# Kernel optimization log

Measured on AMD Instinct MI355X. Metric: run time of the kernel, lower is better.

The kernel has to match this reference:

```python
import jax, jax.numpy as jnp
import numpy as np

DIM = 4096
K = 16  # 2**bits, bits=4
SCALE = 1.0 / DIM ** 0.5
# Lloyd-Max optimal 16-level quantizer centroids for N(0,1)
LLOYD_MAX_4BIT = np.array([
    -2.7326, -2.0690, -1.6181, -1.2562, -0.9424, -0.6568, -0.3881, -0.1284,
     0.1284,  0.3881,  0.6568,  0.9424,  1.2562,  1.6181,  2.0690,  2.7326,
], dtype=np.float32)


def setup_inputs() -> dict:
    key = jax.random.key(0)
    k_x, k_q = jax.random.split(key)
    x = jax.random.normal(k_x, (2048, DIM), dtype=jnp.float32)
    # Random orthogonal rotation via QR, matching torch.linalg.qr(randn(dim, dim))
    g = jax.random.normal(k_q, (DIM, DIM), dtype=jnp.float32)
    rotation, _ = jnp.linalg.qr(g)
    codebook = jnp.asarray(LLOYD_MAX_4BIT)
    return {"x": x, "rotation": rotation, "codebook": codebook}


def reference(x, rotation, codebook):
    # x: (N, dim); rotation: (dim, dim) orthogonal; codebook: (K,)
    shape = x.shape
    x_flat = x.reshape(-1, DIM).astype(jnp.float32)
    y = x_flat @ rotation.T                      # (N, dim) rotate
    y_norm = y / SCALE                           # coords ~ N(0, 1)
    # (N, dim, K) distance tensor -> argmin over codebook axis
    dists = jnp.abs(y_norm[..., None] - codebook)
    idx = jnp.argmin(dists, axis=-1)             # (N, dim) int32
    y_hat = codebook[idx] * SCALE                # gather + rescale
    x_hat = y_hat @ rotation                     # inverse rotation
    return x_hat.reshape(shape)
```

## Files before the change

### kernel.cpp

```cpp
#include <hip/hip_runtime.h>
#include <hip/hip_bf16.h>


typedef __attribute__((ext_vector_type(8))) _Float16 f16x8;
typedef __attribute__((ext_vector_type(4))) float f32x4;

__device__ __forceinline__ unsigned short f2h(float f) {
    _Float16 h = (_Float16)f;
    return *reinterpret_cast<unsigned short*>(&h);
}

__device__ __forceinline__ float quant16(float yn, const float* c) {
    float v = c[0];
#pragma unroll
    for (int i = 0; i < 15; i++) {
        const float bnd = 0.5f * (c[i] + c[i + 1]);
        v = (yn > bnd) ? c[i + 1] : v;
    }
    return v;
}

__global__ __launch_bounds__(256) void convert_x_kernel(
    const float* __restrict__ x, unsigned short* __restrict__ xb) {
    const int i = (blockIdx.x * 256 + threadIdx.x) * 4;
    float4 v = *reinterpret_cast<const float4*>(x + i);
    ushort4 b;
    b.x = f2h(v.x); b.y = f2h(v.y); b.z = f2h(v.z); b.w = f2h(v.w);
    *reinterpret_cast<ushort4*>(xb + i) = b;
}

__global__ __launch_bounds__(256) void conv_rot_kernel(
    const float* __restrict__ R, unsigned short* __restrict__ Rb,
    unsigned short* __restrict__ Rt) {
    __shared__ float t[64][65];
    const int tid = threadIdx.x;
    const int tr = blockIdx.y * 64, tc = blockIdx.x * 64;
    const int r0 = tid >> 4;
    const int c4 = (tid & 15) << 2;
#pragma unroll
    for (int i = 0; i < 4; i++) {
        const int r = r0 + i * 16;
        float4 v = *reinterpret_cast<const float4*>(
            &R[(size_t)(tr + r) * 4096 + tc + c4]);
        ushort4 b;
        b.x = f2h(v.x); b.y = f2h(v.y); b.z = f2h(v.z); b.w = f2h(v.w);
        *reinterpret_cast<ushort4*>(&Rb[(size_t)(tr + r) * 4096 + tc + c4]) = b;
        t[r][c4 + 0] = v.x; t[r][c4 + 1] = v.y;
        t[r][c4 + 2] = v.z; t[r][c4 + 3] = v.w;
    }
    __syncthreads();
#pragma unroll
    for (int i = 0; i < 16; i++) {
        const int idx = tid + 256 * i;
        const int rr = idx >> 6;
        const int cc = idx & 63;
        Rt[(size_t)(tc + rr) * 4096 + tr + cc] = f2h(t[cc][rr]);
    }
}

constexpr int GK = 4096;
constexpr int BM = 128, BN = 256, BK = 64;
constexpr int NT = GK / BK;
constexpr int A_LDS = BM * BK * 2;
constexpr int BUF = (BM + BN) * BK * 2;
constexpr int LDS_DYN = 2 * BUF;

template <bool QUANT>
__global__ __launch_bounds__(768, 3) void gemm_nt_kernel(
    const unsigned short* __restrict__ A, const unsigned short* __restrict__ Bt,
    void* __restrict__ Cout, const float* __restrict__ cb16) {
    extern __shared__ char smem[];
    const int tid = threadIdx.x;
    const int lane = tid & 63;
    const int w = tid >> 6;

    const int bid = blockIdx.x;
    const int wgid = (bid & 7) * 32 + (bid >> 3);
    const int tn = wgid & 15;
    const int tm = wgid >> 4;

    if (w >= 8) {
        const int tp = tid - 512;
        const int pw = tp >> 6;
        const int prow = tp >> 3;
        const int pcol = (((tp & 7) ^ (prow & 7)) << 3);
        const unsigned short* P[12];
#pragma unroll
        for (int r = 0; r < 12; r++) {
            const int rir = r * 32 + prow;
            P[r] = (rir < BM)
                ? A + (size_t)(tm * BM + rir) * GK + pcol
                : Bt + (size_t)(tn * BN + (rir - BM)) * GK + pcol;
        }
#pragma unroll
        for (int r = 0; r < 12; r++) {
            __builtin_amdgcn_global_load_lds(
                (const __attribute__((address_space(1))) void*)P[r],
                (__attribute__((address_space(3))) void*)(
                    smem + r * 4096 + pw * 1024), 16, 0, 0);
            P[r] += BK;
        }
        asm volatile("s_waitcnt vmcnt(0)" ::: "memory");
        __builtin_amdgcn_s_barrier();
        __builtin_amdgcn_sched_barrier(0);
        int wb = BUF;
        for (int t = 0; t < NT; ++t) {
            if (t + 1 < NT) {
#pragma unroll
                for (int r = 0; r < 12; r++) {
                    __builtin_amdgcn_global_load_lds(
                        (const __attribute__((address_space(1))) void*)P[r],
                        (__attribute__((address_space(3))) void*)(
                            smem + wb + r * 4096 + pw * 1024), 16, 0, 0);
                    P[r] += BK;
                }
            }
            asm volatile("s_waitcnt vmcnt(0)" ::: "memory");
            __builtin_amdgcn_s_barrier();
            __builtin_amdgcn_sched_barrier(0);
            wb ^= BUF;
        }
        return;
    }

    const int wm = w >> 2;
    const int wn = w & 3;

    f32x4 acc[4][4];
#pragma unroll
    for (int m = 0; m < 4; m++)
#pragma unroll
        for (int n = 0; n < 4; n++) acc[m][n] = (f32x4){0.f, 0.f, 0.f, 0.f};

    const int frow = lane & 15;
    const int sw0 = (((lane >> 4) ^ (frow & 7)) << 4);
    const int sw1 = (((4 + (lane >> 4)) ^ (frow & 7)) << 4);
    const int arow = (wm * 64 + frow) * 128;
    const int brow = A_LDS + (wn * 64 + frow) * 128;

#define LDA(m, sw) (*reinterpret_cast<const f16x8*>(smem + lb + arow + (m) * 2048 + (sw)))
#define LDB(n, sw) (*reinterpret_cast<const f16x8*>(smem + lb + brow + (n) * 2048 + (sw)))
#define MFMA16(A0, A1, A2, A3, B0, B1, B2, B3)                                     \
    acc[0][0] = __builtin_amdgcn_mfma_f32_16x16x32_f16(A0, B0, acc[0][0], 0, 0, 0); \
    acc[0][1] = __builtin_amdgcn_mfma_f32_16x16x32_f16(A0, B1, acc[0][1], 0, 0, 0); \
    acc[0][2] = __builtin_amdgcn_mfma_f32_16x16x32_f16(A0, B2, acc[0][2], 0, 0, 0); \
    acc[0][3] = __builtin_amdgcn_mfma_f32_16x16x32_f16(A0, B3, acc[0][3], 0, 0, 0); \
    acc[1][0] = __builtin_amdgcn_mfma_f32_16x16x32_f16(A1, B0, acc[1][0], 0, 0, 0); \
    acc[1][1] = __builtin_amdgcn_mfma_f32_16x16x32_f16(A1, B1, acc[1][1], 0, 0, 0); \
    acc[1][2] = __builtin_amdgcn_mfma_f32_16x16x32_f16(A1, B2, acc[1][2], 0, 0, 0); \
    acc[1][3] = __builtin_amdgcn_mfma_f32_16x16x32_f16(A1, B3, acc[1][3], 0, 0, 0); \
    acc[2][0] = __builtin_amdgcn_mfma_f32_16x16x32_f16(A2, B0, acc[2][0], 0, 0, 0); \
    acc[2][1] = __builtin_amdgcn_mfma_f32_16x16x32_f16(A2, B1, acc[2][1], 0, 0, 0); \
    acc[2][2] = __builtin_amdgcn_mfma_f32_16x16x32_f16(A2, B2, acc[2][2], 0, 0, 0); \
    acc[2][3] = __builtin_amdgcn_mfma_f32_16x16x32_f16(A2, B3, acc[2][3], 0, 0, 0); \
    acc[3][0] = __builtin_amdgcn_mfma_f32_16x16x32_f16(A3, B0, acc[3][0], 0, 0, 0); \
    acc[3][1] = __builtin_amdgcn_mfma_f32_16x16x32_f16(A3, B1, acc[3][1], 0, 0, 0); \
    acc[3][2] = __builtin_amdgcn_mfma_f32_16x16x32_f16(A3, B2, acc[3][2], 0, 0, 0); \
    acc[3][3] = __builtin_amdgcn_mfma_f32_16x16x32_f16(A3, B3, acc[3][3], 0, 0, 0);

    __builtin_amdgcn_s_barrier();
    __builtin_amdgcn_sched_barrier(0);

    int lb = 0;
    for (int t = 0; t < NT; ++t) {
        f16x8 a00, a01, a02, a03, b00, b01, b02, b03;
        f16x8 a10, a11, a12, a13, b10, b11, b12, b13;
        a00 = LDA(0, sw0); a01 = LDA(1, sw0); a02 = LDA(2, sw0); a03 = LDA(3, sw0);
        b00 = LDB(0, sw0); b01 = LDB(1, sw0); b02 = LDB(2, sw0); b03 = LDB(3, sw0);
        a10 = LDA(0, sw1); a11 = LDA(1, sw1); a12 = LDA(2, sw1); a13 = LDA(3, sw1);
        b10 = LDB(0, sw1); b11 = LDB(1, sw1); b12 = LDB(2, sw1); b13 = LDB(3, sw1);
        asm volatile("s_waitcnt lgkmcnt(8)" ::: "memory");
        __builtin_amdgcn_sched_barrier(0);
        __builtin_amdgcn_s_setprio(1);
        MFMA16(a00, a01, a02, a03, b00, b01, b02, b03)
        __builtin_amdgcn_s_setprio(0);
        asm volatile("s_waitcnt lgkmcnt(0)" ::: "memory");
        __builtin_amdgcn_sched_barrier(0);
        __builtin_amdgcn_s_setprio(1);
        MFMA16(a10, a11, a12, a13, b10, b11, b12, b13)
        __builtin_amdgcn_s_setprio(0);
        __builtin_amdgcn_s_barrier();
        __builtin_amdgcn_sched_barrier(0);
        lb ^= BUF;
    }
#undef LDA
#undef LDB
#undef MFMA16

    const int crow0 = tm * BM + wm * 64 + ((lane >> 4) << 2);
    const int ccol0 = tn * BN + wn * 64 + frow;
    if constexpr (QUANT) {
        float c[16];
#pragma unroll
        for (int i = 0; i < 16; i++) c[i] = cb16[i];
        unsigned short* O = (unsigned short*)Cout;
#pragma unroll
        for (int m = 0; m < 4; m++)
#pragma unroll
            for (int n = 0; n < 4; n++)
#pragma unroll
                for (int j = 0; j < 4; j++)
                    O[(size_t)(crow0 + m * 16 + j) * 4096 + ccol0 + n * 16] =
                        f2h(quant16(acc[m][n][j] * 64.0f, c) * 0.015625f);
    } else {
        float* O = (float*)Cout;
#pragma unroll
        for (int m = 0; m < 4; m++)
#pragma unroll
            for (int n = 0; n < 4; n++)
#pragma unroll
                for (int j = 0; j < 4; j++)
                    O[(size_t)(crow0 + m * 16 + j) * 4096 + ccol0 + n * 16] =
                        acc[m][n][j];
    }
}

extern "C" void kernel_launch(void* const* d_in, const int* in_sizes, int n_in,
                              void* d_out, int out_size, void* d_ws,
                              size_t ws_size, hipStream_t stream) {
    const float* x = (const float*)d_in[0];
    const float* rot = (const float*)d_in[1];
    const float* cb = (const float*)d_in[2];
    float* out = (float*)d_out;

    unsigned short* Xh = (unsigned short*)d_ws;
    unsigned short* Rh = Xh + (size_t)2048 * 4096;
    unsigned short* Rt = Rh + (size_t)4096 * 4096;
    unsigned short* Yh = Rt + (size_t)4096 * 4096;

    (void)hipFuncSetAttribute(
        reinterpret_cast<const void*>(&gemm_nt_kernel<true>),
        hipFuncAttributeMaxDynamicSharedMemorySize, LDS_DYN);
    (void)hipFuncSetAttribute(
        reinterpret_cast<const void*>(&gemm_nt_kernel<false>),
        hipFuncAttributeMaxDynamicSharedMemorySize, LDS_DYN);

    convert_x_kernel<<<8192, 256, 0, stream>>>(x, Xh);
    conv_rot_kernel<<<dim3(64, 64), 256, 0, stream>>>(rot, Rh, Rt);
    gemm_nt_kernel<true><<<256, 768, LDS_DYN, stream>>>(Xh, Rh, (void*)Yh, cb);
    gemm_nt_kernel<false><<<256, 768, LDS_DYN, stream>>>(Yh, Rt, (void*)out, nullptr);
}
```

Before: 170.0 us.

## Triple-buffer LDS stages and prefetch next tile's fragments across barrier

The producer waves now keep two K-tiles in flight using three LDS buffers instead of two. The consumer waves load the first half-fragments of the next tile into registers before the barrier, so LDS read latency overlaps with MFMA work. This raises dynamic LDS use by half, to about 144KB per block, which may limit occupancy under the 3-block launch bound. It also adds register pressure from the extra fragment sets.

```diff
diff --git a/kernel.cpp b/kernel.cpp
--- a/kernel.cpp
+++ b/kernel.cpp
@@ -63,7 +63,7 @@
 constexpr int NT = GK / BK;
 constexpr int A_LDS = BM * BK * 2;
 constexpr int BUF = (BM + BN) * BK * 2;
-constexpr int LDS_DYN = 2 * BUF;
+constexpr int LDS_DYN = 3 * BUF;
 
 template <bool QUANT>
 __global__ __launch_bounds__(768, 3) void gemm_nt_kernel(
@@ -92,34 +92,31 @@
                 ? A + (size_t)(tm * BM + rir) * GK + pcol
                 : Bt + (size_t)(tn * BN + (rir - BM)) * GK + pcol;
         }
-#pragma unroll
-        for (int r = 0; r < 12; r++) {
-            __builtin_amdgcn_global_load_lds(
-                (const __attribute__((address_space(1))) void*)P[r],
-                (__attribute__((address_space(3))) void*)(
-                    smem + r * 4096 + pw * 1024), 16, 0, 0);
-            P[r] += BK;
+#define PSTAGE(dstbase)                                                        \
+        {                                                                      \
+            _Pragma("unroll")                                                  \
+            for (int r = 0; r < 12; r++) {                                     \
+                __builtin_amdgcn_global_load_lds(                              \
+                    (const __attribute__((address_space(1))) void*)P[r],       \
+                    (__attribute__((address_space(3))) void*)(                 \
+                        smem + (dstbase) + r * 4096 + pw * 1024), 16, 0, 0);   \
+                P[r] += BK;                                                    \
+            }                                                                  \
         }
+        PSTAGE(0)
+        PSTAGE(BUF)
         asm volatile("s_waitcnt vmcnt(0)" ::: "memory");
         __builtin_amdgcn_s_barrier();
         __builtin_amdgcn_sched_barrier(0);
-        int wb = BUF;
+        int wb = 2 * BUF;
         for (int t = 0; t < NT; ++t) {
-            if (t + 1 < NT) {
-#pragma unroll
-                for (int r = 0; r < 12; r++) {
-                    __builtin_amdgcn_global_load_lds(
-                        (const __attribute__((address_space(1))) void*)P[r],
-                        (__attribute__((address_space(3))) void*)(
-                            smem + wb + r * 4096 + pw * 1024), 16, 0, 0);
-                    P[r] += BK;
-                }
-            }
+            if (t + 2 < NT) PSTAGE(wb)
             asm volatile("s_waitcnt vmcnt(0)" ::: "memory");
             __builtin_amdgcn_s_barrier();
             __builtin_amdgcn_sched_barrier(0);
-            wb ^= BUF;
+            wb = (wb == 2 * BUF) ? 0 : wb + BUF;
         }
+#undef PSTAGE
         return;
     }
 
@@ -138,8 +135,8 @@
     const int arow = (wm * 64 + frow) * 128;
     const int brow = A_LDS + (wn * 64 + frow) * 128;
 
-#define LDA(m, sw) (*reinterpret_cast<const f16x8*>(smem + lb + arow + (m) * 2048 + (sw)))
-#define LDB(n, sw) (*reinterpret_cast<const f16x8*>(smem + lb + brow + (n) * 2048 + (sw)))
+#define LDA(base, m, sw) (*reinterpret_cast<const f16x8*>(smem + (base) + arow + (m) * 2048 + (sw)))
+#define LDB(base, n, sw) (*reinterpret_cast<const f16x8*>(smem + (base) + brow + (n) * 2048 + (sw)))
 #define MFMA16(A0, A1, A2, A3, B0, B1, B2, B3)                                     \
     acc[0][0] = __builtin_amdgcn_mfma_f32_16x16x32_f16(A0, B0, acc[0][0], 0, 0, 0); \
     acc[0][1] = __builtin_amdgcn_mfma_f32_16x16x32_f16(A0, B1, acc[0][1], 0, 0, 0); \
@@ -158,31 +155,52 @@
     acc[3][2] = __builtin_amdgcn_mfma_f32_16x16x32_f16(A3, B2, acc[3][2], 0, 0, 0); \
     acc[3][3] = __builtin_amdgcn_mfma_f32_16x16x32_f16(A3, B3, acc[3][3], 0, 0, 0);
 
+    f16x8 Pa0, Pa1, Pa2, Pa3, Pb0, Pb1, Pb2, Pb3;
+    f16x8 Qa0, Qa1, Qa2, Qa3, Qb0, Qb1, Qb2, Qb3;
+    f16x8 Ra0, Ra1, Ra2, Ra3, Rb0, Rb1, Rb2, Rb3;
+
+#define LOADSET(S, base, sw)                                                   \
+    S##a0 = LDA(base, 0, sw); S##a1 = LDA(base, 1, sw);                        \
+    S##a2 = LDA(base, 2, sw); S##a3 = LDA(base, 3, sw);                        \
+    S##b0 = LDB(base, 0, sw); S##b1 = LDB(base, 1, sw);                        \
+    S##b2 = LDB(base, 2, sw); S##b3 = LDB(base, 3, sw);
+
     __builtin_amdgcn_s_barrier();
     __builtin_amdgcn_sched_barrier(0);
-
-    int lb = 0;
-    for (int t = 0; t < NT; ++t) {
-        f16x8 a00, a01, a02, a03, b00, b01, b02, b03;
-        f16x8 a10, a11, a12, a13, b10, b11, b12, b13;
-        a00 = LDA(0, sw0); a01 = LDA(1, sw0); a02 = LDA(2, sw0); a03 = LDA(3, sw0);
-        b00 = LDB(0, sw0); b01 = LDB(1, sw0); b02 = LDB(2, sw0); b03 = LDB(3, sw0);
-        a10 = LDA(0, sw1); a11 = LDA(1, sw1); a12 = LDA(2, sw1); a13 = LDA(3, sw1);
-        b10 = LDB(0, sw1); b11 = LDB(1, sw1); b12 = LDB(2, sw1); b13 = LDB(3, sw1);
-        asm volatile("s_waitcnt lgkmcnt(8)" ::: "memory");
-        __builtin_amdgcn_sched_barrier(0);
-        __builtin_amdgcn_s_setprio(1);
-        MFMA16(a00, a01, a02, a03, b00, b01, b02, b03)
-        __builtin_amdgcn_s_setprio(0);
-        asm volatile("s_waitcnt lgkmcnt(0)" ::: "memory");
-        __builtin_amdgcn_sched_barrier(0);
-        __builtin_amdgcn_s_setprio(1);
-        MFMA16(a10, a11, a12, a13, b10, b11, b12, b13)
-        __builtin_amdgcn_s_setprio(0);
-        __builtin_amdgcn_s_barrier();
-        __builtin_amdgcn_sched_barrier(0);
-        lb ^= BUF;
-    }
+    int lb0 = 0, lb1 = BUF;
+    LOADSET(P, 0, sw0)
+
+#define CBODY(CUR, NXT, t)                                                     \
+    {                                                                          \
+        LOADSET(R, lb0, sw1)                              \
+        asm volatile("s_waitcnt lgkmcnt(8)" ::: "memory");    \
+        __builtin_amdgcn_sched_barrier(0);                                     \
+        __builtin_amdgcn_s_setprio(1);                                         \
+        MFMA16(CUR##a0, CUR##a1, CUR##a2, CUR##a3,                             \
+               CUR##b0, CUR##b1, CUR##b2, CUR##b3)                             \
+        __builtin_amdgcn_s_setprio(0);                                         \
+        if ((t) + 1 < NT) {                                                    \
+            LOADSET(NXT, lb1, sw0)                      \
+            asm volatile("s_waitcnt lgkmcnt(8)" ::: "memory");     \
+        } else {                                                               \
+            asm volatile("s_waitcnt lgkmcnt(0)" ::: "memory");                 \
+        }                                                                      \
+        __builtin_amdgcn_sched_barrier(0);                                     \
+        __builtin_amdgcn_s_setprio(1);                                         \
+        MFMA16(Ra0, Ra1, Ra2, Ra3, Rb0, Rb1, Rb2, Rb3)                         \
+        __builtin_amdgcn_s_setprio(0);                                         \
+        __builtin_amdgcn_s_barrier();                                          \
+        __builtin_amdgcn_sched_barrier(0);                                     \
+        lb0 = lb1;                                                             \
+        lb1 = (lb1 == 2 * BUF) ? 0 : lb1 + BUF;                                \
+    }
+
+    for (int t = 0; t < NT; t += 2) {
+        CBODY(P, Q, t)
+        CBODY(Q, P, t + 1)
+    }
+#undef CBODY
+#undef LOADSET
 #undef LDA
 #undef LDB
 #undef MFMA16
```

Result: slower. 418.4 us (+146.1%).
